# Performance work log

Hardware: AMD Instinct MI355X
Metric: run time of the kernel (lower is better)

## Reference

```python
import jax, jax.numpy as jnp
import numpy as np

N = 131072   # total utterances (nodes)
B = 2048     # conversations (segments)
F = 200      # n_features (hard-coded 200 in source)
STEPS = 3    # processing_steps (reason_steps[0])


def setup_inputs() -> dict:
    key = jax.random.key(0)
    k = jax.random.split(key, 8)
    x = jax.random.normal(k[0], (N, F), dtype=jnp.float32)
    batch = jnp.sort(jax.random.randint(k[1], (N,), 0, B, dtype=jnp.int32))
    cos_coef = jax.random.normal(k[2], (N,), dtype=jnp.float32)
    q_star = jax.random.normal(k[3], (B, 2 * F), dtype=jnp.float32)
    s = 1.0 / np.sqrt(F)
    # PyTorch LSTM params: gate order i, f, g, o; input size 2F, hidden F
    W_ih = jax.random.uniform(k[4], (4 * F, 2 * F), jnp.float32, -s, s)
    W_hh = jax.random.uniform(k[5], (4 * F, F), jnp.float32, -s, s)
    b_ih = jax.random.uniform(k[6], (4 * F,), jnp.float32, -s, s)
    b_hh = jax.random.uniform(k[7], (4 * F,), jnp.float32, -s, s)
    return {"x": x, "batch": batch, "cos_coef": cos_coef, "q_star": q_star,
            "W_ih": W_ih, "W_hh": W_hh, "b_ih": b_ih, "b_hh": b_hh}


def _lstm_cell(inp, h, c, W_ih, W_hh, b_ih, b_hh):
    gates = inp @ W_ih.T + b_ih + h @ W_hh.T + b_hh  # [B, 4F]
    i, f, g, o = jnp.split(gates, 4, axis=-1)
    c = jax.nn.sigmoid(f) * c + jax.nn.sigmoid(i) * jnp.tanh(g)
    h = jax.nn.sigmoid(o) * jnp.tanh(c)
    return h, c


def reference(x, batch, cos_coef, q_star, W_ih, W_hh, b_ih, b_hh):
    # initial LSTM hidden: a_sit[i] = cos_row_i @ x[segment_i]  -> segment_sum
    h = jax.ops.segment_sum(cos_coef[:, None] * x, batch, num_segments=B)  # [B,F]
    c = jnp.zeros((B, F), dtype=x.dtype)
    for _ in range(STEPS):
        h, c = _lstm_cell(q_star, h, c, W_ih, W_hh, b_ih, b_hh)
        q = h                                            # [B,F]
        e = jnp.sum(x * q[batch], axis=-1)               # [N]
        m = jax.ops.segment_max(e, batch, num_segments=B)
        ex = jnp.exp(e - m[batch])
        denom = jax.ops.segment_sum(ex, batch, num_segments=B)
        a = ex / denom[batch]                            # per-segment softmax
        r = jax.ops.segment_sum(a[:, None] * x, batch, num_segments=B)  # [B,F]
        q_star = jnp.concatenate([q, r], axis=-1)        # [B,2F]
    return q_star
```

## Files before the change

kernel.cpp:

```cpp
#include <hip/hip_runtime.h>
#include <hip/hip_bf16.h>

#define N_NODES 131072
#define B_SEG   2048
#define F_DIM   200
#define K_DIM   608
#define NEG_INF (-3.4e38f)

typedef __attribute__((ext_vector_type(8))) short bf16x8;
typedef __attribute__((ext_vector_type(4))) float f32x4;

__device__ __forceinline__ float b2f(unsigned short u) {
  union { unsigned int i; float f; } v; v.i = ((unsigned int)u) << 16; return v.f;
}
__device__ __forceinline__ unsigned short f2bu(float f) {
  __hip_bfloat16 h = __float2bfloat16(f);
  return *reinterpret_cast<unsigned short*>(&h);
}
__device__ __forceinline__ float sigmoidf_(float x) { return 1.f / (1.f + __expf(-x)); }

__global__ __launch_bounds__(256) void setup_kernel(
    const float* __restrict__ Wih, const float* __restrict__ Whh,
    const float* __restrict__ bih, const float* __restrict__ bhh,
    const int* __restrict__ batch, unsigned short* __restrict__ Wc,
    float* __restrict__ bsum, int* __restrict__ seg_off) {
  int bid = blockIdx.x, tid = threadIdx.x;
  if (bid < 1976) {
    int idx = bid * 256 + tid;
    int row = idx / K_DIM, k = idx - row * K_DIM;
    float v = 0.f;
    if (row < 800) {
      if (k < 400)      v = Wih[row * 400 + k];
      else if (k < 600) v = Whh[row * 200 + (k - 400)];
    }
    Wc[idx] = f2bu(v);
  } else if (bid < 1976 + 512) {
    int i = (bid - 1976) * 256 + tid;
    int v  = batch[i];
    int pv = (i == 0) ? -1 : batch[i - 1];
    for (int b = pv + 1; b <= v; b++) seg_off[b] = i;
  } else {
    int idx = (bid - 2488) * 256 + tid;
    if (idx < 800) bsum[idx] = bih[idx] + bhh[idx];
    else if (idx == 800) {
      int last = batch[N_NODES - 1];
      for (int b = last + 1; b <= B_SEG; b++) seg_off[b] = N_NODES;
    }
  }
}

__global__ __launch_bounds__(256) void init_kernel(
    const float* __restrict__ xf, const int* __restrict__ seg_off,
    const float* __restrict__ cosc, const float* __restrict__ qs0,
    unsigned short* __restrict__ xb, unsigned short* __restrict__ A) {
  __shared__ float rpart[4][F_DIM];
  int b = blockIdx.x, tid = threadIdx.x;
  int start = seg_off[b], end = seg_off[b + 1];
  int n = end - start;
  unsigned short* Arow = A + (size_t)b * K_DIM;
  int wave = tid >> 6, lane = tid & 63;
  float a0 = 0.f, a1 = 0.f, a2 = 0.f, a3 = 0.f;
  for (int r = wave; r < n; r += 4) {
    if (lane < 50) {
      float4 v = *(const float4*)(xf + (size_t)(start + r) * F_DIM + 4 * lane);
      ushort4 o; o.x = f2bu(v.x); o.y = f2bu(v.y); o.z = f2bu(v.z); o.w = f2bu(v.w);
      *(ushort4*)(xb + (size_t)(start + r) * F_DIM + 4 * lane) = o;
      float cv = cosc[start + r];
      a0 += cv * b2f(o.x); a1 += cv * b2f(o.y);
      a2 += cv * b2f(o.z); a3 += cv * b2f(o.w);
    }
  }
  if (lane < 50) {
    rpart[wave][4 * lane]     = a0;
    rpart[wave][4 * lane + 1] = a1;
    rpart[wave][4 * lane + 2] = a2;
    rpart[wave][4 * lane + 3] = a3;
  }
  for (int j = tid; j < 400; j += 256)
    Arow[j] = f2bu(qs0[(size_t)b * 400 + j]);
  if (tid < 8) Arow[600 + tid] = 0;
  __syncthreads();
  if (tid < F_DIM) {
    float acc = rpart[0][tid] + rpart[1][tid] + rpart[2][tid] + rpart[3][tid];
    Arow[400 + tid] = f2bu(acc);
  }
}

__global__ __launch_bounds__(256) void gemm_gates(
    const unsigned short* __restrict__ A, const unsigned short* __restrict__ W,
    float* __restrict__ gates) {
  int tid = threadIdx.x;
  int bm = blockIdx.x * 64, bn = blockIdx.y * 64;
  int wave = tid >> 6, lane = tid & 63;
  int quad = lane >> 4, col = lane & 15;
  f32x4 acc[4];
#pragma unroll
  for (int t = 0; t < 4; t++) acc[t] = (f32x4){0.f, 0.f, 0.f, 0.f};
  const unsigned short* Ap = A + (size_t)(bm + wave * 16 + col) * K_DIM + quad * 8;
  const unsigned short* Wp = W + (size_t)(bn + col) * K_DIM + quad * 8;
#pragma unroll
  for (int k0 = 0; k0 < K_DIM; k0 += 32) {
    bf16x8 af = *(const bf16x8*)(Ap + k0);
#pragma unroll
    for (int t = 0; t < 4; t++) {
      bf16x8 bfr = *(const bf16x8*)(Wp + (size_t)t * 16 * K_DIM + k0);
      acc[t] = __builtin_amdgcn_mfma_f32_16x16x32_bf16(af, bfr, acc[t], 0, 0, 0);
    }
  }
#pragma unroll
  for (int t = 0; t < 4; t++) {
    int gn = bn + t * 16 + col;
    if (gn < 800) {
#pragma unroll
      for (int r = 0; r < 4; r++) {
        int gm = bm + wave * 16 + quad * 4 + r;
        gates[(size_t)gm * 800 + gn] = acc[t][r];
      }
    }
  }
}

__global__ __launch_bounds__(256) void attn_fused(
    const unsigned short* __restrict__ xb, const int* __restrict__ seg_off,
    const float* __restrict__ gates, const float* __restrict__ bsum,
    float* __restrict__ cvec, unsigned short* __restrict__ A,
    float* __restrict__ out, int step) {
  __shared__ float q_s[F_DIM];
  __shared__ float rpart[4][F_DIM];
  __shared__ float red[8];
  int b = blockIdx.x, tid = threadIdx.x;
  int start = seg_off[b], end = seg_off[b + 1];
  int n = end - start;
  unsigned short* Arow = A + (size_t)b * K_DIM;
  if (tid < F_DIM) {
    int f = tid;
    const float* g = gates + (size_t)b * 800;
    float gi = g[f]       + bsum[f];
    float gf = g[200 + f] + bsum[200 + f];
    float gg = g[400 + f] + bsum[400 + f];
    float go = g[600 + f] + bsum[600 + f];
    float cp = (step > 0) ? cvec[(size_t)b * F_DIM + f] : 0.f;
    float cn = sigmoidf_(gf) * cp + sigmoidf_(gi) * tanhf(gg);
    float hn = sigmoidf_(go) * tanhf(cn);
    cvec[(size_t)b * F_DIM + f] = cn;
    q_s[f] = hn;
    if (step < 2) {
      unsigned short hb = f2bu(hn);
      Arow[f] = hb;
      Arow[400 + f] = hb;
    }
  }
  __syncthreads();
  int wave = tid >> 6, lane = tid & 63;
  float q0 = 0.f, q1 = 0.f, q2 = 0.f, q3 = 0.f;
  if (lane < 50) {
    q0 = q_s[4 * lane];     q1 = q_s[4 * lane + 1];
    q2 = q_s[4 * lane + 2]; q3 = q_s[4 * lane + 3];
  }
  const unsigned short* xrow = xb + (size_t)start * F_DIM + 4 * lane;
  float m = NEG_INF, l = 0.f;
  float a0 = 0.f, a1 = 0.f, a2 = 0.f, a3 = 0.f;
  for (int r = wave; r < n; r += 4) {
    float x0 = 0.f, x1 = 0.f, x2 = 0.f, x3 = 0.f;
    float p = 0.f;
    if (lane < 50) {
      ushort4 v = *(const ushort4*)(xrow + (size_t)r * F_DIM);
      x0 = b2f(v.x); x1 = b2f(v.y); x2 = b2f(v.z); x3 = b2f(v.w);
      p = q0 * x0 + q1 * x1 + q2 * x2 + q3 * x3;
    }
#pragma unroll
    for (int off = 32; off; off >>= 1) p += __shfl_down(p, off);
    float e = __shfl(p, 0);
    float mn = fmaxf(m, e);
    float fac = __expf(m - mn);
    float w  = __expf(e - mn);
    l  = l * fac + w;
    a0 = a0 * fac + w * x0;  a1 = a1 * fac + w * x1;
    a2 = a2 * fac + w * x2;  a3 = a3 * fac + w * x3;
    m = mn;
  }
  if (lane == 0) red[wave] = m;
  __syncthreads();
  float M = fmaxf(fmaxf(red[0], red[1]), fmaxf(red[2], red[3]));
  float facw = (m > NEG_INF) ? __expf(m - M) : 0.f;
  if (lane == 0) red[4 + wave] = l * facw;
  if (lane < 50) {
    rpart[wave][4 * lane]     = a0 * facw;
    rpart[wave][4 * lane + 1] = a1 * facw;
    rpart[wave][4 * lane + 2] = a2 * facw;
    rpart[wave][4 * lane + 3] = a3 * facw;
  }
  __syncthreads();
  float L = red[4] + red[5] + red[6] + red[7];
  float inv = (L > 0.f) ? 1.f / L : 0.f;
  if (tid < F_DIM) {
    float rv = (rpart[0][tid] + rpart[1][tid] + rpart[2][tid] + rpart[3][tid]) * inv;
    if (step < 2) {
      Arow[200 + tid] = f2bu(rv);
    } else {
      out[(size_t)b * 400 + tid]       = q_s[tid];
      out[(size_t)b * 400 + 200 + tid] = rv;
    }
  }
}

extern "C" void kernel_launch(void* const* d_in, const int* in_sizes, int n_in,
                              void* d_out, int out_size, void* d_ws, size_t ws_size,
                              hipStream_t stream) {
  const float* x    = (const float*)d_in[0];
  const int*   batch= (const int*)d_in[1];
  const float* cosc = (const float*)d_in[2];
  const float* qs0  = (const float*)d_in[3];
  const float* Wih  = (const float*)d_in[4];
  const float* Whh  = (const float*)d_in[5];
  const float* bih  = (const float*)d_in[6];
  const float* bhh  = (const float*)d_in[7];
  char* ws = (char*)d_ws;
  unsigned short* xb   = (unsigned short*)(ws);
  unsigned short* A    = (unsigned short*)(ws + 52428800);
  unsigned short* Wc   = (unsigned short*)(ws + 54919168);
  float*          gates= (float*)(ws + 55930880);
  float*          cvec = (float*)(ws + 62484480);
  float*          bsum = (float*)(ws + 64122880);
  int*            soff = (int*)(ws + 64126080);
  float*          outp = (float*)d_out;

  setup_kernel<<<2492, 256, 0, stream>>>(Wih, Whh, bih, bhh, batch, Wc, bsum, soff);
  init_kernel<<<B_SEG, 256, 0, stream>>>(x, soff, cosc, qs0, xb, A);
  for (int s = 0; s < 3; s++) {
    gemm_gates<<<dim3(32, 13), 256, 0, stream>>>(A, Wc, gates);
    attn_fused<<<B_SEG, 256, 0, stream>>>(xb, soff, gates, bsum, cvec, A, outp, s);
  }
}
```

Baseline: 287.9 us.

## Raise lane utilization in init, attention and gate GEMM kernels

The init kernel now maps 250 threads onto five row groups of 50 float4 columns, and vectorizes the q_star copy, so fewer lanes sit idle. The attention kernel splits each wave into two half-waves that each process one row with 16-byte loads, giving eight rows in flight per block and a shorter 32-lane shuffle reduction. The gate GEMM halves the M tile to 32 rows and doubles the grid, so more blocks spread across compute units. In exchange there are more shared-memory partials, more registers per thread, and W fragments are loaded redundantly across more blocks.

```diff
diff --git a/kernel.cpp b/kernel.cpp
--- a/kernel.cpp
+++ b/kernel.cpp
@@ -53,35 +53,37 @@
     const float* __restrict__ xf, const int* __restrict__ seg_off,
     const float* __restrict__ cosc, const float* __restrict__ qs0,
     unsigned short* __restrict__ xb, unsigned short* __restrict__ A) {
-  __shared__ float rpart[4][F_DIM];
+  __shared__ float rpart[5][F_DIM];
   int b = blockIdx.x, tid = threadIdx.x;
   int start = seg_off[b], end = seg_off[b + 1];
   int n = end - start;
   unsigned short* Arow = A + (size_t)b * K_DIM;
-  int wave = tid >> 6, lane = tid & 63;
+  int rgrp = tid / 50, col4 = tid - rgrp * 50;
   float a0 = 0.f, a1 = 0.f, a2 = 0.f, a3 = 0.f;
-  for (int r = wave; r < n; r += 4) {
-    if (lane < 50) {
-      float4 v = *(const float4*)(xf + (size_t)(start + r) * F_DIM + 4 * lane);
+  if (rgrp < 5) {
+    for (int r = rgrp; r < n; r += 5) {
+      float4 v = *(const float4*)(xf + (size_t)(start + r) * F_DIM + 4 * col4);
       ushort4 o; o.x = f2bu(v.x); o.y = f2bu(v.y); o.z = f2bu(v.z); o.w = f2bu(v.w);
-      *(ushort4*)(xb + (size_t)(start + r) * F_DIM + 4 * lane) = o;
+      *(ushort4*)(xb + (size_t)(start + r) * F_DIM + 4 * col4) = o;
       float cv = cosc[start + r];
       a0 += cv * b2f(o.x); a1 += cv * b2f(o.y);
       a2 += cv * b2f(o.z); a3 += cv * b2f(o.w);
     }
-  }
-  if (lane < 50) {
-    rpart[wave][4 * lane]     = a0;
-    rpart[wave][4 * lane + 1] = a1;
-    rpart[wave][4 * lane + 2] = a2;
-    rpart[wave][4 * lane + 3] = a3;
-  }
-  for (int j = tid; j < 400; j += 256)
-    Arow[j] = f2bu(qs0[(size_t)b * 400 + j]);
+    rpart[rgrp][4 * col4]     = a0;
+    rpart[rgrp][4 * col4 + 1] = a1;
+    rpart[rgrp][4 * col4 + 2] = a2;
+    rpart[rgrp][4 * col4 + 3] = a3;
+  }
+  if (tid < 100) {
+    float4 v = *(const float4*)(qs0 + (size_t)b * 400 + 4 * tid);
+    ushort4 o; o.x = f2bu(v.x); o.y = f2bu(v.y); o.z = f2bu(v.z); o.w = f2bu(v.w);
+    *(ushort4*)(Arow + 4 * tid) = o;
+  }
   if (tid < 8) Arow[600 + tid] = 0;
   __syncthreads();
   if (tid < F_DIM) {
-    float acc = rpart[0][tid] + rpart[1][tid] + rpart[2][tid] + rpart[3][tid];
+    float acc = rpart[0][tid] + rpart[1][tid] + rpart[2][tid] + rpart[3][tid]
+              + rpart[4][tid];
     Arow[400 + tid] = f2bu(acc);
   }
 }
@@ -90,30 +92,32 @@
     const unsigned short* __restrict__ A, const unsigned short* __restrict__ W,
     float* __restrict__ gates) {
   int tid = threadIdx.x;
-  int bm = blockIdx.x * 64, bn = blockIdx.y * 64;
+  int bm = blockIdx.x * 32, bn = blockIdx.y * 64;
   int wave = tid >> 6, lane = tid & 63;
   int quad = lane >> 4, col = lane & 15;
-  f32x4 acc[4];
-#pragma unroll
-  for (int t = 0; t < 4; t++) acc[t] = (f32x4){0.f, 0.f, 0.f, 0.f};
-  const unsigned short* Ap = A + (size_t)(bm + wave * 16 + col) * K_DIM + quad * 8;
+  int strip = wave >> 1;
+  int tp = (wave & 1) * 2;
+  f32x4 acc[2];
+  acc[0] = (f32x4){0.f, 0.f, 0.f, 0.f};
+  acc[1] = (f32x4){0.f, 0.f, 0.f, 0.f};
+  const unsigned short* Ap = A + (size_t)(bm + strip * 16 + col) * K_DIM + quad * 8;
   const unsigned short* Wp = W + (size_t)(bn + col) * K_DIM + quad * 8;
 #pragma unroll
   for (int k0 = 0; k0 < K_DIM; k0 += 32) {
     bf16x8 af = *(const bf16x8*)(Ap + k0);
 #pragma unroll
-    for (int t = 0; t < 4; t++) {
-      bf16x8 bfr = *(const bf16x8*)(Wp + (size_t)t * 16 * K_DIM + k0);
+    for (int t = 0; t < 2; t++) {
+      bf16x8 bfr = *(const bf16x8*)(Wp + (size_t)(tp + t) * 16 * K_DIM + k0);
       acc[t] = __builtin_amdgcn_mfma_f32_16x16x32_bf16(af, bfr, acc[t], 0, 0, 0);
     }
   }
 #pragma unroll
-  for (int t = 0; t < 4; t++) {
-    int gn = bn + t * 16 + col;
+  for (int t = 0; t < 2; t++) {
+    int gn = bn + (tp + t) * 16 + col;
     if (gn < 800) {
 #pragma unroll
       for (int r = 0; r < 4; r++) {
-        int gm = bm + wave * 16 + quad * 4 + r;
+        int gm = bm + strip * 16 + quad * 4 + r;
         gates[(size_t)gm * 800 + gn] = acc[t][r];
       }
     }
@@ -126,8 +130,8 @@
     float* __restrict__ cvec, unsigned short* __restrict__ A,
     float* __restrict__ out, int step) {
   __shared__ float q_s[F_DIM];
-  __shared__ float rpart[4][F_DIM];
-  __shared__ float red[8];
+  __shared__ float rpart[8][F_DIM];
+  __shared__ float redm[8], redl[8];
   int b = blockIdx.x, tid = threadIdx.x;
   int start = seg_off[b], end = seg_off[b + 1];
   int n = end - start;
@@ -152,49 +156,56 @@
   }
   __syncthreads();
   int wave = tid >> 6, lane = tid & 63;
-  float q0 = 0.f, q1 = 0.f, q2 = 0.f, q3 = 0.f;
-  if (lane < 50) {
-    q0 = q_s[4 * lane];     q1 = q_s[4 * lane + 1];
-    q2 = q_s[4 * lane + 2]; q3 = q_s[4 * lane + 3];
-  }
-  const unsigned short* xrow = xb + (size_t)start * F_DIM + 4 * lane;
+  int half = lane >> 5, hl = lane & 31;
+  int hw = wave * 2 + half;
+  bool act = (hl < 25);
+  float q0=0,q1=0,q2=0,q3=0,q4=0,q5=0,q6=0,q7=0;
+  if (act) {
+    q0 = q_s[8*hl];   q1 = q_s[8*hl+1]; q2 = q_s[8*hl+2]; q3 = q_s[8*hl+3];
+    q4 = q_s[8*hl+4]; q5 = q_s[8*hl+5]; q6 = q_s[8*hl+6]; q7 = q_s[8*hl+7];
+  }
+  const unsigned short* xp = xb + (size_t)start * F_DIM + 8 * hl;
   float m = NEG_INF, l = 0.f;
-  float a0 = 0.f, a1 = 0.f, a2 = 0.f, a3 = 0.f;
-  for (int r = wave; r < n; r += 4) {
-    float x0 = 0.f, x1 = 0.f, x2 = 0.f, x3 = 0.f;
+  float a0=0,a1=0,a2=0,a3=0,a4=0,a5=0,a6=0,a7=0;
+  for (int r = hw; r < n; r += 8) {
+    float x0=0,x1=0,x2=0,x3=0,x4=0,x5=0,x6=0,x7=0;
     float p = 0.f;
-    if (lane < 50) {
-      ushort4 v = *(const ushort4*)(xrow + (size_t)r * F_DIM);
-      x0 = b2f(v.x); x1 = b2f(v.y); x2 = b2f(v.z); x3 = b2f(v.w);
-      p = q0 * x0 + q1 * x1 + q2 * x2 + q3 * x3;
-    }
-#pragma unroll
-    for (int off = 32; off; off >>= 1) p += __shfl_down(p, off);
-    float e = __shfl(p, 0);
+    if (act) {
+      uint4 v = *(const uint4*)(xp + (size_t)r * F_DIM);
+      x0 = b2f((unsigned short)(v.x & 0xffff)); x1 = b2f((unsigned short)(v.x >> 16));
+      x2 = b2f((unsigned short)(v.y & 0xffff)); x3 = b2f((unsigned short)(v.y >> 16));
+      x4 = b2f((unsigned short)(v.z & 0xffff)); x5 = b2f((unsigned short)(v.z >> 16));
+      x6 = b2f((unsigned short)(v.w & 0xffff)); x7 = b2f((unsigned short)(v.w >> 16));
+      p = q0*x0 + q1*x1 + q2*x2 + q3*x3 + q4*x4 + q5*x5 + q6*x6 + q7*x7;
+    }
+#pragma unroll
+    for (int off = 16; off; off >>= 1) p += __shfl_xor(p, off, 32);
+    float e = p;
     float mn = fmaxf(m, e);
     float fac = __expf(m - mn);
     float w  = __expf(e - mn);
     l  = l * fac + w;
-    a0 = a0 * fac + w * x0;  a1 = a1 * fac + w * x1;
-    a2 = a2 * fac + w * x2;  a3 = a3 * fac + w * x3;
+    a0 = a0*fac + w*x0; a1 = a1*fac + w*x1; a2 = a2*fac + w*x2; a3 = a3*fac + w*x3;
+    a4 = a4*fac + w*x4; a5 = a5*fac + w*x5; a6 = a6*fac + w*x6; a7 = a7*fac + w*x7;
     m = mn;
   }
-  if (lane == 0) red[wave] = m;
-  __syncthreads();
-  float M = fmaxf(fmaxf(red[0], red[1]), fmaxf(red[2], red[3]));
+  if (hl == 0) redm[hw] = m;
+  __syncthreads();
+  float M = fmaxf(fmaxf(fmaxf(redm[0], redm[1]), fmaxf(redm[2], redm[3])),
+                  fmaxf(fmaxf(redm[4], redm[5]), fmaxf(redm[6], redm[7])));
   float facw = (m > NEG_INF) ? __expf(m - M) : 0.f;
-  if (lane == 0) red[4 + wave] = l * facw;
-  if (lane < 50) {
-    rpart[wave][4 * lane]     = a0 * facw;
-    rpart[wave][4 * lane + 1] = a1 * facw;
-    rpart[wave][4 * lane + 2] = a2 * facw;
-    rpart[wave][4 * lane + 3] = a3 * facw;
-  }
-  __syncthreads();
-  float L = red[4] + red[5] + red[6] + red[7];
+  if (hl == 0) redl[hw] = l * facw;
+  if (act) {
+    float* rp = &rpart[hw][8 * hl];
+    rp[0] = a0*facw; rp[1] = a1*facw; rp[2] = a2*facw; rp[3] = a3*facw;
+    rp[4] = a4*facw; rp[5] = a5*facw; rp[6] = a6*facw; rp[7] = a7*facw;
+  }
+  __syncthreads();
+  float L = redl[0]+redl[1]+redl[2]+redl[3]+redl[4]+redl[5]+redl[6]+redl[7];
   float inv = (L > 0.f) ? 1.f / L : 0.f;
   if (tid < F_DIM) {
-    float rv = (rpart[0][tid] + rpart[1][tid] + rpart[2][tid] + rpart[3][tid]) * inv;
+    float rv = (rpart[0][tid]+rpart[1][tid]+rpart[2][tid]+rpart[3][tid]
+              + rpart[4][tid]+rpart[5][tid]+rpart[6][tid]+rpart[7][tid]) * inv;
     if (step < 2) {
       Arow[200 + tid] = f2bu(rv);
     } else {
@@ -228,7 +239,7 @@
   setup_kernel<<<2492, 256, 0, stream>>>(Wih, Whh, bih, bhh, batch, Wc, bsum, soff);
   init_kernel<<<B_SEG, 256, 0, stream>>>(x, soff, cosc, qs0, xb, A);
   for (int s = 0; s < 3; s++) {
-    gemm_gates<<<dim3(32, 13), 256, 0, stream>>>(A, Wc, gates);
+    gemm_gates<<<dim3(64, 13), 256, 0, stream>>>(A, Wc, gates);
     attn_fused<<<B_SEG, 256, 0, stream>>>(xb, soff, gates, bsum, cvec, A, outp, s);
   }
 }
```

Result: faster. 275.4 us (-4.3%).
